# Optimization experiments

Measured on AMD Instinct MI355X. Metric: run time of the kernel, lower is better.

Reference implementation:

```python
import jax, jax.numpy as jnp
import numpy as np

N_NODES = 50000
N_EDGES = 800000
IN_DIM = 128
OUT_DIM = 64
HEADS = 8
HEAD_DIM = OUT_DIM // HEADS
NEG_SLOPE = 0.2


def setup_inputs() -> dict:
    key = jax.random.key(0)
    k1, k2, k3, k4, k5 = jax.random.split(key, 5)
    x = jax.random.normal(k1, (N_NODES, IN_DIM), dtype=jnp.float32)
    edge_indices = jax.random.randint(k2, (2, N_EDGES), 0, N_NODES, dtype=jnp.int64)
    # Linear(input_dim, output_dim, bias=False): weight is [out, in]
    W = jax.random.normal(k3, (OUT_DIM, IN_DIM), dtype=jnp.float32) * (1.0 / np.sqrt(IN_DIM))
    src_attn = jax.random.normal(k4, (HEADS, HEAD_DIM), dtype=jnp.float32) * (1.0 / np.sqrt(HEAD_DIM))
    dst_attn = jax.random.normal(k5, (HEADS, HEAD_DIM), dtype=jnp.float32) * (1.0 / np.sqrt(HEAD_DIM))
    return {"x": x, "edge_indices": edge_indices, "W": W, "src_attn": src_attn, "dst_attn": dst_attn}


def reference(x, edge_indices, W, src_attn, dst_attn):
    # Eval mode: all dropouts are identity.
    N = x.shape[0]
    # add self loops
    loops = jnp.arange(N, dtype=edge_indices.dtype)
    ei = jnp.concatenate([edge_indices, jnp.stack([loops, loops])], axis=1)  # [2, E+N]
    row, col = ei[0], ei[1]

    h = (x @ W.T).reshape(N, HEADS, HEAD_DIM)  # [N, H, D]
    s = jnp.einsum("nhd,hd->nh", h, src_attn)  # [N, H]
    d = jnp.einsum("nhd,hd->nh", h, dst_attn)  # [N, H]

    e = jax.nn.leaky_relu(s[row] + d[col], negative_slope=NEG_SLOPE)  # [E', H]

    # segment softmax over rows (torch.sparse.softmax with dim=1 normalizes per row)
    m = jax.ops.segment_max(e, row, num_segments=N)          # [N, H]
    ex = jnp.exp(e - m[row])                                 # [E', H]
    denom = jax.ops.segment_sum(ex, row, num_segments=N)    # [N, H]
    w = ex / denom[row]                                      # [E', H]

    # sparse.mm per head: out[row] += w * h[col]
    msg = w[:, :, None] * h[col]                             # [E', H, D]
    out = jax.ops.segment_sum(msg, row, num_segments=N)      # [N, H, D]
    return out.reshape(N, HEADS * HEAD_DIM)
```

## Files before the change

kernel.cpp:

```cpp
#include <hip/hip_runtime.h>

#define NN 50000
#define IN_DIM 128
#define OUT_DIM 64
#define HEADS 8
#define NEG_SLOPE 0.2f
#define LOG2E 1.44269504088896340736f

#define GEMM_NB ((NN + 63) / 64)
#define NBUCK 196
#define CAP 6144

typedef __bf16 bf16x8 __attribute__((ext_vector_type(8)));
typedef float f32x4 __attribute__((ext_vector_type(4)));

static __device__ __forceinline__ unsigned short f2bf(float f) {
    __bf16 b = (__bf16)f;
    return __builtin_bit_cast(unsigned short, b);
}
static __device__ __forceinline__ float bf2f(unsigned short u) {
    return __uint_as_float(((unsigned)u) << 16);
}

static __device__ __forceinline__ int detect_i64(const int* __restrict__ ei,
                                                 int lane) {
    unsigned long long b = __ballot(ei[2 * lane + 1] != 0);
    return (b == 0ull) ? 1 : 0;
}

__global__ __launch_bounds__(256) void k_fused0(
        const float* __restrict__ x, const float* __restrict__ W,
        const float* __restrict__ sa, const float* __restrict__ da,
        const int* __restrict__ ei,
        unsigned short* __restrict__ hb, float* __restrict__ s,
        float* __restrict__ d, int* __restrict__ bucketCount,
        unsigned* __restrict__ tmp, int E) {
    __shared__ int hist[NBUCK];
    const int tid  = threadIdx.x;
    const int lane = tid & 63;

    if (blockIdx.x >= GEMM_NB) {
        const int bx = blockIdx.x - GEMM_NB;
        if (tid < NBUCK) hist[tid] = 0;
        const int f = detect_i64(ei, lane);
        __syncthreads();

        const int base = bx * 2048 + tid * 8;
        int rw[8], cl[8];
        const bool fullvec = (base + 8 <= E) && ((E & 3) == 0);
        if (f) {
            if (fullvec) {
                const int4* p = (const int4*)(ei + 2 * base);
                const int4* q = (const int4*)(ei + 2 * E + 2 * base);
                #pragma unroll
                for (int g = 0; g < 4; ++g) {
                    int4 a = p[g]; int4 b = q[g];
                    rw[2 * g] = a.x; rw[2 * g + 1] = a.z;
                    cl[2 * g] = b.x; cl[2 * g + 1] = b.z;
                }
            } else {
                #pragma unroll
                for (int k = 0; k < 8; ++k) {
                    int e = base + k;
                    rw[k] = (e < E) ? ei[2 * e] : -1;
                    cl[k] = (e < E) ? ei[2 * E + 2 * e] : 0;
                }
            }
        } else {
            if (fullvec) {
                const int4* p = (const int4*)(ei + base);
                const int4* q = (const int4*)(ei + E + base);
                int4 a0 = p[0], a1 = p[1], b0 = q[0], b1 = q[1];
                rw[0] = a0.x; rw[1] = a0.y; rw[2] = a0.z; rw[3] = a0.w;
                rw[4] = a1.x; rw[5] = a1.y; rw[6] = a1.z; rw[7] = a1.w;
                cl[0] = b0.x; cl[1] = b0.y; cl[2] = b0.z; cl[3] = b0.w;
                cl[4] = b1.x; cl[5] = b1.y; cl[6] = b1.z; cl[7] = b1.w;
            } else {
                #pragma unroll
                for (int k = 0; k < 8; ++k) {
                    int e = base + k;
                    rw[k] = (e < E) ? ei[e] : -1;
                    cl[k] = (e < E) ? ei[E + e] : 0;
                }
            }
        }

        #pragma unroll
        for (int k = 0; k < 8; ++k)
            if (rw[k] >= 0) atomicAdd(&hist[rw[k] >> 8], 1);
        __syncthreads();
        if (tid < NBUCK) {
            int c = hist[tid];
            int b0 = (c > 0) ? atomicAdd(&bucketCount[tid], c) : 0;
            hist[tid] = tid * CAP + b0;
        }
        __syncthreads();
        #pragma unroll
        for (int k = 0; k < 8; ++k) {
            if (rw[k] >= 0) {
                int bk = rw[k] >> 8;
                int pos = atomicAdd(&hist[bk], 1);
                if (pos < (bk + 1) * CAP)
                    tmp[pos] = ((unsigned)(rw[k] & 255) << 24) | (unsigned)cl[k];
            }
        }
        return;
    }

    const int wave = tid >> 6;
    const int c    = lane & 15;
    const int kg   = lane >> 4;
    const int n0   = blockIdx.x * 64 + wave * 16;

    bf16x8 bf[4][4];
    #pragma unroll
    for (int kt = 0; kt < 4; ++kt) {
        #pragma unroll
        for (int ot = 0; ot < 4; ++ot) {
            const float* wp = &W[(ot * 16 + c) * 128 + kt * 32 + kg * 8];
            f32x4 w0 = *(const f32x4*)wp;
            f32x4 w1 = *(const f32x4*)(wp + 4);
            bf16x8 b;
            #pragma unroll
            for (int j = 0; j < 4; ++j) { b[j] = (__bf16)w0[j]; b[4 + j] = (__bf16)w1[j]; }
            bf[kt][ot] = b;
        }
    }

    int nr = n0 + c; if (nr > NN - 1) nr = NN - 1;
    const float* xp = &x[(long)nr * 128 + kg * 8];

    f32x4 acc[4] = {};
    #pragma unroll
    for (int kt = 0; kt < 4; ++kt) {
        f32x4 x0 = *(const f32x4*)(xp + kt * 32);
        f32x4 x1 = *(const f32x4*)(xp + kt * 32 + 4);
        bf16x8 a;
        #pragma unroll
        for (int j = 0; j < 4; ++j) { a[j] = (__bf16)x0[j]; a[4 + j] = (__bf16)x1[j]; }
        #pragma unroll
        for (int ot = 0; ot < 4; ++ot)
            acc[ot] = __builtin_amdgcn_mfma_f32_16x16x32_bf16(a, bf[kt][ot], acc[ot], 0, 0, 0);
    }

    float sav[4], dav[4];
    #pragma unroll
    for (int ot = 0; ot < 4; ++ot) {
        sav[ot] = sa[ot * 16 + c] * LOG2E;
        dav[ot] = da[ot * 16 + c] * LOG2E;
    }

    const int nodebase = n0 + kg * 4;
    #pragma unroll
    for (int r = 0; r < 4; ++r) {
        const int n = nodebase + r;
        const bool ok = (n < NN);
        if (ok) {
            #pragma unroll
            for (int ot = 0; ot < 4; ++ot) hb[n * 64 + ot * 16 + c] = f2bf(acc[ot][r]);
        }
        float ps[4], pd[4];
        #pragma unroll
        for (int ot = 0; ot < 4; ++ot) { ps[ot] = acc[ot][r] * sav[ot]; pd[ot] = acc[ot][r] * dav[ot]; }
        #pragma unroll
        for (int m = 1; m < 8; m <<= 1) {
            #pragma unroll
            for (int ot = 0; ot < 4; ++ot) {
                ps[ot] += __shfl_xor(ps[ot], m, 64);
                pd[ot] += __shfl_xor(pd[ot], m, 64);
            }
        }
        if (ok && (c & 7) == 0) {
            const int hbid = c >> 3;
            #pragma unroll
            for (int ot = 0; ot < 4; ++ot) {
                s[n * 8 + 2 * ot + hbid] = ps[ot];
                d[n * 8 + 2 * ot + hbid] = pd[ot];
            }
        }
    }
}

__global__ __launch_bounds__(256) void k_sort2(
        const unsigned* __restrict__ tmp, const int* __restrict__ bucketCount,
        int2* __restrict__ offsse, int* __restrict__ scol) {
    __shared__ int bins[256];
    __shared__ int pref[256];
    const int d = blockIdx.x, t = threadIdx.x;
    const int base = d * CAP;
    int cnt = bucketCount[d]; if (cnt > CAP) cnt = CAP;
    const int end = base + cnt;

    bins[t] = 0;
    __syncthreads();
    for (int i = base + t; i < end; i += 256)
        atomicAdd(&bins[tmp[i] >> 24], 1);
    __syncthreads();

    const int bv = bins[t];
    pref[t] = bv;
    __syncthreads();
    for (int off = 1; off < 256; off <<= 1) {
        int u = (t >= off) ? pref[t - off] : 0;
        __syncthreads();
        pref[t] += u;
        __syncthreads();
    }
    const int incl = pref[t];
    const int excl = incl - bv;

    const int row = d * 256 + t;
    if (row < NN) offsse[row] = make_int2(base + excl, base + incl);

    bins[t] = excl;
    __syncthreads();
    for (int i = base + t; i < end; i += 256) {
        unsigned v = tmp[i];
        int p = atomicAdd(&bins[v >> 24], 1);
        scol[base + p] = (int)(v & 0xFFFFFF);
    }
}

__global__ __launch_bounds__(256) void k_gather(
        const unsigned short* __restrict__ hb, const float* __restrict__ s,
        const float* __restrict__ d, const int2* __restrict__ offsse,
        const int* __restrict__ scol, float* __restrict__ out) {
    const int tid  = threadIdx.x;
    const int n    = blockIdx.x * 4 + (tid >> 6);
    const int lane = tid & 63;
    const int o    = lane;
    const int oh   = o >> 3;
    const int eidx = lane >> 3;
    const int h    = lane & 7;

    const float sn_h = s[n * 8 + h];

    const int2 se   = offsse[n];
    const int b     = se.x;
    const int e_end = se.y;

    float acc  = 0.0f;
    float dsum = 0.0f;

    for (int i = b; i < e_end; i += 8) {
        const int myi  = i + eidx;
        const bool val = (myi < e_end);
        int addr = val ? myi : (e_end - 1);
        int c = scol[addr];
        float dv = d[c * 8 + h];
        float v = sn_h + dv;
        v = fmaxf(v, NEG_SLOPE * v);
        v = val ? v : -10000.0f;
        float ev = __builtin_amdgcn_exp2f(v);
        dsum += ev;

        #pragma unroll
        for (int k = 0; k < 8; ++k) {
            int   c_k = __builtin_amdgcn_readlane(c, k * 8);
            float e_k = __shfl(ev, k * 8 + oh);
            acc += e_k * bf2f(hb[c_k * 64 + o]);
        }
    }

    dsum += __shfl_xor(dsum, 8, 64);
    dsum += __shfl_xor(dsum, 16, 64);
    dsum += __shfl_xor(dsum, 32, 64);
    float denom = __shfl(dsum, oh);

    const float sn_o = s[n * 8 + oh];
    const float dn_o = d[n * 8 + oh];
    float vs = sn_o + dn_o;
    vs = fmaxf(vs, NEG_SLOPE * vs);
    const float es = __builtin_amdgcn_exp2f(vs);
    denom += es;
    acc += es * bf2f(hb[n * 64 + o]);

    out[n * 64 + o] = acc / denom;
}

extern "C" void kernel_launch(void* const* d_in, const int* in_sizes, int n_in,
                              void* d_out, int out_size, void* d_ws, size_t ws_size,
                              hipStream_t stream) {
    const float* x  = (const float*)d_in[0];
    const int*   ei = (const int*)d_in[1];
    const float* W  = (const float*)d_in[2];
    const float* sa = (const float*)d_in[3];
    const float* da = (const float*)d_in[4];
    float* out = (float*)d_out;
    const int E = in_sizes[1] / 2;

    const int NB1 = (E + 2047) / 2048;

    unsigned short* hb = (unsigned short*)d_ws;
    float* s    = (float*)(hb + NN * 64);
    float* dd   = s + NN * 8;
    int2*  offsse = (int2*)(dd + NN * 8);
    int*   bucketCount = (int*)(offsse + NN);
    unsigned* tmp = (unsigned*)(bucketCount + NBUCK + 2);
    int*   scol = (int*)(tmp + NBUCK * CAP);

    hipMemsetAsync(bucketCount, 0, NBUCK * sizeof(int), stream);
    k_fused0<<<GEMM_NB + NB1, 256, 0, stream>>>(x, W, sa, da, ei,
                                                hb, s, dd, bucketCount, tmp, E);
    k_sort2<<<NBUCK, 256, 0, stream>>>(tmp, bucketCount, offsse, scol);
    k_gather<<<NN / 4, 256, 0, stream>>>(hb, s, dd, offsse, scol, out);
}
```

Baseline: 77.08 us.

## Fuse bucket sort into gather kernel and stage scatter through LDS

Merges the per-bucket counting sort with the attention gather into one kernel. Each of two blocks per bucket re-sorts the bucket's records into shared memory, then processes half of the bucket's rows, which removes the scol/offsse global round trip and one launch. The binning stage now builds a block-local prefix sum and writes records in bucket order through LDS, so global scatter writes are coalesced. In exchange the sort work is done twice per bucket, only 392 large blocks run the gather, and 1024-thread blocks with about 26KB of LDS may limit occupancy.

```diff
diff --git a/kernel.cpp b/kernel.cpp
--- a/kernel.cpp
+++ b/kernel.cpp
@@ -10,6 +10,7 @@
 #define GEMM_NB ((NN + 63) / 64)
 #define NBUCK 196
 #define CAP 6144
+#define SPLIT 2
 
 typedef __bf16 bf16x8 __attribute__((ext_vector_type(8)));
 typedef float f32x4 __attribute__((ext_vector_type(4)));
@@ -36,6 +37,11 @@
         float* __restrict__ d, int* __restrict__ bucketCount,
         unsigned* __restrict__ tmp, int E) {
     __shared__ int hist[NBUCK];
+    __shared__ int lpre[NBUCK];
+    __shared__ int gbase[NBUCK];
+    __shared__ int pref[256];
+    __shared__ unsigned lrec[2048];
+    __shared__ int tot_s;
     const int tid  = threadIdx.x;
     const int lane = tid & 63;
 
@@ -89,20 +95,43 @@
         for (int k = 0; k < 8; ++k)
             if (rw[k] >= 0) atomicAdd(&hist[rw[k] >> 8], 1);
         __syncthreads();
+
+        int myCnt = (tid < NBUCK) ? hist[tid] : 0;
+        pref[tid] = myCnt;
+        __syncthreads();
+        for (int off = 1; off < 256; off <<= 1) {
+            int u = (tid >= off) ? pref[tid - off] : 0;
+            __syncthreads();
+            pref[tid] += u;
+            __syncthreads();
+        }
         if (tid < NBUCK) {
-            int c = hist[tid];
-            int b0 = (c > 0) ? atomicAdd(&bucketCount[tid], c) : 0;
-            hist[tid] = tid * CAP + b0;
-        }
-        __syncthreads();
+            int ex = pref[tid] - myCnt;
+            lpre[tid]  = ex;
+            gbase[tid] = tid * CAP + ((myCnt > 0) ? atomicAdd(&bucketCount[tid], myCnt) : 0);
+            hist[tid]  = ex;
+        }
+        if (tid == 255) tot_s = pref[255];
+        __syncthreads();
+
         #pragma unroll
         for (int k = 0; k < 8; ++k) {
             if (rw[k] >= 0) {
                 int bk = rw[k] >> 8;
-                int pos = atomicAdd(&hist[bk], 1);
-                if (pos < (bk + 1) * CAP)
-                    tmp[pos] = ((unsigned)(rw[k] & 255) << 24) | (unsigned)cl[k];
-            }
+                int lp = atomicAdd(&hist[bk], 1);
+                lrec[lp] = ((unsigned)rw[k] << 16) | (unsigned)cl[k];
+            }
+        }
+        __syncthreads();
+
+        const int tot = tot_s;
+        for (int j = tid; j < tot; j += 256) {
+            unsigned v = lrec[j];
+            int row = (int)(v >> 16);
+            int bk  = row >> 8;
+            int pos = gbase[bk] + (j - lpre[bk]);
+            if (pos < (bk + 1) * CAP)
+                tmp[pos] = ((unsigned)(row & 255) << 24) | (v & 0xFFFFu);
         }
         return;
     }
@@ -181,101 +210,97 @@
     }
 }
 
-__global__ __launch_bounds__(256) void k_sort2(
+__global__ __launch_bounds__(1024) void k_bgather(
         const unsigned* __restrict__ tmp, const int* __restrict__ bucketCount,
-        int2* __restrict__ offsse, int* __restrict__ scol) {
+        const unsigned short* __restrict__ hb, const float* __restrict__ sarr,
+        const float* __restrict__ d, float* __restrict__ out) {
     __shared__ int bins[256];
     __shared__ int pref[256];
-    const int d = blockIdx.x, t = threadIdx.x;
-    const int base = d * CAP;
-    int cnt = bucketCount[d]; if (cnt > CAP) cnt = CAP;
-    const int end = base + cnt;
-
-    bins[t] = 0;
-    __syncthreads();
-    for (int i = base + t; i < end; i += 256)
-        atomicAdd(&bins[tmp[i] >> 24], 1);
-    __syncthreads();
-
-    const int bv = bins[t];
-    pref[t] = bv;
+    __shared__ int lcol[CAP];
+    const int t    = threadIdx.x;
+    const int bkt  = blockIdx.x >> 1;
+    const int half = blockIdx.x & 1;
+    const int base = bkt * CAP;
+    int cnt = bucketCount[bkt]; if (cnt > CAP) cnt = CAP;
+
+    if (t < 256) bins[t] = 0;
+    __syncthreads();
+    for (int i = t; i < cnt; i += 1024)
+        atomicAdd(&bins[tmp[base + i] >> 24], 1);
+    __syncthreads();
+
+    if (t < 256) pref[t] = bins[t];
     __syncthreads();
     for (int off = 1; off < 256; off <<= 1) {
-        int u = (t >= off) ? pref[t - off] : 0;
-        __syncthreads();
-        pref[t] += u;
-        __syncthreads();
-    }
-    const int incl = pref[t];
-    const int excl = incl - bv;
-
-    const int row = d * 256 + t;
-    if (row < NN) offsse[row] = make_int2(base + excl, base + incl);
-
-    bins[t] = excl;
-    __syncthreads();
-    for (int i = base + t; i < end; i += 256) {
-        unsigned v = tmp[i];
+        int u = 0;
+        if (t < 256 && t >= off) u = pref[t - off];
+        __syncthreads();
+        if (t < 256) pref[t] += u;
+        __syncthreads();
+    }
+    if (t < 256) bins[t] = pref[t] - bins[t];
+    __syncthreads();
+    for (int i = t; i < cnt; i += 1024) {
+        unsigned v = tmp[base + i];
         int p = atomicAdd(&bins[v >> 24], 1);
-        scol[base + p] = (int)(v & 0xFFFFFF);
-    }
-}
-
-__global__ __launch_bounds__(256) void k_gather(
-        const unsigned short* __restrict__ hb, const float* __restrict__ s,
-        const float* __restrict__ d, const int2* __restrict__ offsse,
-        const int* __restrict__ scol, float* __restrict__ out) {
-    const int tid  = threadIdx.x;
-    const int n    = blockIdx.x * 4 + (tid >> 6);
-    const int lane = tid & 63;
+        lcol[p] = (int)(v & 0xFFFFFF);
+    }
+    __syncthreads();
+
+    const int lane = t & 63;
+    const int wid  = t >> 6;
     const int o    = lane;
     const int oh   = o >> 3;
     const int eidx = lane >> 3;
     const int h    = lane & 7;
 
-    const float sn_h = s[n * 8 + h];
-
-    const int2 se   = offsse[n];
-    const int b     = se.x;
-    const int e_end = se.y;
-
-    float acc  = 0.0f;
-    float dsum = 0.0f;
-
-    for (int i = b; i < e_end; i += 8) {
-        const int myi  = i + eidx;
-        const bool val = (myi < e_end);
-        int addr = val ? myi : (e_end - 1);
-        int c = scol[addr];
-        float dv = d[c * 8 + h];
-        float v = sn_h + dv;
-        v = fmaxf(v, NEG_SLOPE * v);
-        v = val ? v : -10000.0f;
-        float ev = __builtin_amdgcn_exp2f(v);
-        dsum += ev;
-
-        #pragma unroll
-        for (int k = 0; k < 8; ++k) {
-            int   c_k = __builtin_amdgcn_readlane(c, k * 8);
-            float e_k = __shfl(ev, k * 8 + oh);
-            acc += e_k * bf2f(hb[c_k * 64 + o]);
-        }
-    }
-
-    dsum += __shfl_xor(dsum, 8, 64);
-    dsum += __shfl_xor(dsum, 16, 64);
-    dsum += __shfl_xor(dsum, 32, 64);
-    float denom = __shfl(dsum, oh);
-
-    const float sn_o = s[n * 8 + oh];
-    const float dn_o = d[n * 8 + oh];
-    float vs = sn_o + dn_o;
-    vs = fmaxf(vs, NEG_SLOPE * vs);
-    const float es = __builtin_amdgcn_exp2f(vs);
-    denom += es;
-    acc += es * bf2f(hb[n * 64 + o]);
-
-    out[n * 64 + o] = acc / denom;
+    #pragma unroll
+    for (int rr = 0; rr < 256 / (16 * SPLIT); ++rr) {
+        const int rl = half * 128 + rr * 16 + wid;
+        const int n  = bkt * 256 + rl;
+        if (n >= NN) continue;
+
+        const int bgn = (rl == 0) ? 0 : pref[rl - 1];
+        const int end = pref[rl];
+
+        const float sn_h = sarr[n * 8 + h];
+        float acc  = 0.0f;
+        float dsum = 0.0f;
+
+        for (int i = bgn; i < end; i += 8) {
+            const int myi  = i + eidx;
+            const bool val = (myi < end);
+            int c = lcol[val ? myi : (end - 1)];
+            float dv = d[c * 8 + h];
+            float v = sn_h + dv;
+            v = fmaxf(v, NEG_SLOPE * v);
+            v = val ? v : -10000.0f;
+            float ev = __builtin_amdgcn_exp2f(v);
+            dsum += ev;
+
+            #pragma unroll
+            for (int k = 0; k < 8; ++k) {
+                int   c_k = __builtin_amdgcn_readlane(c, k * 8);
+                float e_k = __shfl(ev, k * 8 + oh);
+                acc += e_k * bf2f(hb[c_k * 64 + o]);
+            }
+        }
+
+        dsum += __shfl_xor(dsum, 8, 64);
+        dsum += __shfl_xor(dsum, 16, 64);
+        dsum += __shfl_xor(dsum, 32, 64);
+        float denom = __shfl(dsum, oh);
+
+        const float sn_o = sarr[n * 8 + oh];
+        const float dn_o = d[n * 8 + oh];
+        float vs = sn_o + dn_o;
+        vs = fmaxf(vs, NEG_SLOPE * vs);
+        const float es = __builtin_amdgcn_exp2f(vs);
+        denom += es;
+        acc += es * bf2f(hb[n * 64 + o]);
+
+        out[n * 64 + o] = acc / denom;
+    }
 }
 
 extern "C" void kernel_launch(void* const* d_in, const int* in_sizes, int n_in,
@@ -294,14 +319,11 @@
     unsigned short* hb = (unsigned short*)d_ws;
     float* s    = (float*)(hb + NN * 64);
     float* dd   = s + NN * 8;
-    int2*  offsse = (int2*)(dd + NN * 8);
-    int*   bucketCount = (int*)(offsse + NN);
-    unsigned* tmp = (unsigned*)(bucketCount + NBUCK + 2);
-    int*   scol = (int*)(tmp + NBUCK * CAP);
+    int*   bucketCount = (int*)(dd + NN * 8);
+    unsigned* tmp = (unsigned*)(bucketCount + NBUCK + 4);
 
     hipMemsetAsync(bucketCount, 0, NBUCK * sizeof(int), stream);
     k_fused0<<<GEMM_NB + NB1, 256, 0, stream>>>(x, W, sa, da, ei,
                                                 hb, s, dd, bucketCount, tmp, E);
-    k_sort2<<<NBUCK, 256, 0, stream>>>(tmp, bucketCount, offsse, scol);
-    k_gather<<<NN / 4, 256, 0, stream>>>(hb, s, dd, offsse, scol, out);
-}
+    k_bgather<<<NBUCK * SPLIT, 1024, 0, stream>>>(tmp, bucketCount, hb, s, dd, out);
+}
```

Measured after the change: 74.25 us. 3.7% less time.
